# Performance work log

Hardware: AMD Instinct MI355X
Metric: run time of the kernel (lower is better)

Reference implementation:

```python
import jax, jax.numpy as jnp
import numpy as np

HEADS = 8
DIM_HEAD = 64


def setup_inputs() -> dict:
    key = jax.random.key(0)
    ks = jax.random.split(key, 7)
    b, c, h, w = 8, 256, 64, 64
    hidden = HEADS * DIM_HEAD  # 512
    return {
        "x": jax.random.normal(ks[0], (b, c, h, w), dtype=jnp.float32),
        "context": jax.random.normal(ks[1], (b, c, h, w), dtype=jnp.float32),
        "Wq": jax.random.normal(ks[2], (hidden, c), dtype=jnp.float32) * 0.02,
        "Wk": jax.random.normal(ks[3], (hidden, c), dtype=jnp.float32) * 0.02,
        "Wv": jax.random.normal(ks[4], (hidden, c), dtype=jnp.float32) * 0.02,
        "Wo": jax.random.normal(ks[5], (c, hidden), dtype=jnp.float32) * 0.02,
        "bo": jnp.zeros((c,), dtype=jnp.float32),
    }


def reference(x, context, Wq, Wk, Wv, Wo, bo):
    b, c, h, w = x.shape
    n = h * w
    scale = DIM_HEAD ** (-0.5)
    xf = x.reshape(b, c, n)                      # b c n
    cf = context.reshape(b, context.shape[1], -1)  # b c m
    # 1x1 convs == per-pixel linear projections
    q = jnp.einsum('bcn,oc->bon', xf, Wq).reshape(b, HEADS, DIM_HEAD, n) * scale
    k = jnp.einsum('bcm,oc->bom', cf, Wk).reshape(b, HEADS, DIM_HEAD, -1)
    v = jnp.einsum('bcm,oc->bom', cf, Wv).reshape(b, HEADS, DIM_HEAD, -1)
    k = jax.nn.softmax(k, axis=-1)               # softmax over spatial positions
    ctx = jnp.einsum('bhdm,bhem->bhde', k, v)    # small d x e context
    out = jnp.einsum('bhde,bhdn->bhen', ctx, q)  # b h e n
    out = out.reshape(b, HEADS * DIM_HEAD, h, w)
    return jnp.einsum('bchw,oc->bohw', out, Wo) + bo[None, :, None, None]
```

## Files before the change

### kernel.cpp

```cpp
#include <hip/hip_runtime.h>

#define B   8
#define C   256
#define N   4096
#define H   8
#define D   64
#define HID 512
#define SCALE 0.125f

typedef __attribute__((ext_vector_type(8))) __bf16 bf16x8;
typedef __attribute__((ext_vector_type(4))) float f32x4;

__device__ __forceinline__ ushort f2bf(float f) {
  union { float f; unsigned u; } v; v.f = f;
  unsigned r = v.u + 0x7FFFu + ((v.u >> 16) & 1u);
  return (ushort)(r >> 16);
}

__device__ __forceinline__ f32x4 mfma16(bf16x8 a, bf16x8 b, f32x4 c) {
  return __builtin_amdgcn_mfma_f32_16x16x32_bf16(a, b, c, 0, 0, 0);
}

__global__ __launch_bounds__(256) void cast_w_kernel(
    const float* __restrict__ Wk, const float* __restrict__ Wv,
    ushort* __restrict__ wk_bf, ushort* __restrict__ wv_bf) {
  const int t = (blockIdx.x * 256 + threadIdx.x) * 4;
  const float4 a = *(const float4*)(Wk + t);
  const float4 b = *(const float4*)(Wv + t);
  ushort4 ra, rb;
  ra.x = f2bf(a.x); ra.y = f2bf(a.y); ra.z = f2bf(a.z); ra.w = f2bf(a.w);
  rb.x = f2bf(b.x); rb.y = f2bf(b.y); rb.z = f2bf(b.z); rb.w = f2bf(b.w);
  *(ushort4*)(wk_bf + t) = ra;
  *(ushort4*)(wv_bf + t) = rb;
}

__global__ __launch_bounds__(256) void transpose_cast_kernel(
    const float* __restrict__ src, ushort* __restrict__ dst, int R, int L) {
  __shared__ float tile[64 * 65];
  const int l0 = blockIdx.x * 64, r0 = blockIdx.y * 64, b = blockIdx.z;
  const int tid = threadIdx.x;
  const int rr = tid >> 4, c4 = (tid & 15) << 2;
  const float* sp = src + ((size_t)b * R + r0) * L + l0;
#pragma unroll
  for (int p = 0; p < 4; ++p) {
    const float4 v = *(const float4*)(sp + (size_t)(rr + p * 16) * L + c4);
    float* tp = tile + (rr + p * 16) * 65 + c4;
    tp[0] = v.x; tp[1] = v.y; tp[2] = v.z; tp[3] = v.w;
  }
  __syncthreads();
  const int lr = tid >> 2, rb = (tid & 3) << 4;
  uint pk[8];
#pragma unroll
  for (int k = 0; k < 16; k += 2) {
    const uint lo = f2bf(tile[(rb + k) * 65 + lr]);
    const uint hi = f2bf(tile[(rb + k + 1) * 65 + lr]);
    pk[k >> 1] = lo | (hi << 16);
  }
  ushort* dp = dst + ((size_t)b * L + l0 + lr) * R + r0 + rb;
  *(uint4*)dp = *(uint4*)pk;
  *(uint4*)(dp + 8) = *(uint4*)(pk + 4);
}

__global__ __launch_bounds__(256, 3) void kv_mfma_kernel(
    const ushort* __restrict__ ctxt_bf,
    const ushort* __restrict__ wk_bf,
    const ushort* __restrict__ wv_bf,
    float* __restrict__ ctx_part,
    float* __restrict__ z_part)
{
  __shared__ __align__(16) ushort cb_s[64 * 256];
  __shared__ __align__(16) ushort p_s[64 * 64];
  __shared__ __align__(16) ushort v_s[64 * 64];
  const int mt = blockIdx.x, h = blockIdx.y, b = blockIdx.z;
  const int tid = threadIdx.x;
  const int w = tid >> 6, lane = tid & 63;
  const int col = lane & 15, quad = lane >> 4;
  const int dw = w * 16;
  const int c7 = col & 7;

  const ushort* wkp = wk_bf + (size_t)(h * 64 + dw + col) * C + quad * 8;
  const ushort* wvp = wv_bf + (size_t)(h * 64 + dw + col) * C + quad * 8;

  const int sgcol = lane & 31;
  const int srowo = w * 16 + (lane >> 5);

  const f32x4 z4 = {0.f, 0.f, 0.f, 0.f};
  f32x4 cacc[4];
#pragma unroll
  for (int j = 0; j < 4; ++j) cacc[j] = z4;
  float zl = 0.f;

  for (int mh = 0; mh < 4; ++mh) {
    const size_t m0 = (size_t)mt * 256 + mh * 64;
    const ushort* cbg = ctxt_bf + ((size_t)b * N + m0) * C;

#pragma unroll
    for (int it = 0; it < 8; ++it) {
      const int row = srowo + it * 2;
      const uint4 vld = *(const uint4*)(cbg + (size_t)row * C + sgcol * 8);
      const int gc = sgcol ^ (row & 7);
      *(uint4*)(cb_s + row * 256 + gc * 8) = vld;
    }
    __syncthreads();

    f32x4 kacc[4], vacc[4];
#pragma unroll
    for (int i = 0; i < 4; ++i) { kacc[i] = z4; vacc[i] = z4; }
#pragma unroll
    for (int kc = 0; kc < 2; ++kc) {
      bf16x8 wkf[4], wvf[4];
#pragma unroll
      for (int kk = 0; kk < 4; ++kk) {
        wkf[kk] = *(const bf16x8*)(wkp + (size_t)(kc * 4 + kk) * 32);
        wvf[kk] = *(const bf16x8*)(wvp + (size_t)(kc * 4 + kk) * 32);
      }
#pragma unroll
      for (int kk = 0; kk < 4; ++kk) {
        const int kg = (kc * 4 + kk) * 4 + quad;
        bf16x8 a[4];
#pragma unroll
        for (int i = 0; i < 4; ++i) {
          const int r = i * 16 + col;
          a[i] = *(const bf16x8*)(cb_s + r * 256 + (kg ^ (r & 7)) * 8);
        }
#pragma unroll
        for (int i = 0; i < 4; ++i) {
          kacc[i] = mfma16(a[i], wkf[kk], kacc[i]);
          vacc[i] = mfma16(a[i], wvf[kk], vacc[i]);
        }
      }
    }

#pragma unroll
    for (int i = 0; i < 4; ++i) {
      const int off = (dw + col) * 64 + (((i * 2 + (quad >> 1)) ^ c7) << 3) +
                      ((quad & 1) << 2);
      const f32x4 k4 = kacc[i];
      const float e0 = __expf(k4[0]), e1 = __expf(k4[1]);
      const float e2 = __expf(k4[2]), e3 = __expf(k4[3]);
      zl += (e0 + e1) + (e2 + e3);
      ushort4 pk; pk.x = f2bf(e0); pk.y = f2bf(e1);
      pk.z = f2bf(e2); pk.w = f2bf(e3);
      *(ushort4*)(p_s + off) = pk;
      const f32x4 v4 = vacc[i];
      ushort4 vk; vk.x = f2bf(v4[0]); vk.y = f2bf(v4[1]);
      vk.z = f2bf(v4[2]); vk.w = f2bf(v4[3]);
      *(ushort4*)(v_s + off) = vk;
    }
    __syncthreads();

#pragma unroll
    for (int kq = 0; kq < 2; ++kq) {
      const int gsw = ((kq * 4 + quad) ^ c7) << 3;
      const bf16x8 pa = *(const bf16x8*)(p_s + (dw + col) * 64 + gsw);
      bf16x8 vb[4];
#pragma unroll
      for (int j = 0; j < 4; ++j)
        vb[j] = *(const bf16x8*)(v_s + (j * 16 + col) * 64 + gsw);
#pragma unroll
      for (int j = 0; j < 4; ++j) cacc[j] = mfma16(pa, vb[j], cacc[j]);
    }
  }

  {
    float s = zl;
    s += __shfl_xor(s, 16); s += __shfl_xor(s, 32);
    if (quad == 0)
      z_part[((size_t)(b * H + h) * 16 + mt) * 64 + dw + col] = s;
  }

  float* outp = ctx_part + ((size_t)(b * H + h) * 16 + mt) * 4096;
#pragma unroll
  for (int j = 0; j < 4; ++j)
#pragma unroll
    for (int r = 0; r < 4; ++r)
      outp[(size_t)(dw + quad * 4 + r) * 64 + j * 16 + col] = cacc[j][r];
}

__global__ __launch_bounds__(256) void combine_kernel(
    const float* __restrict__ ctx_part, const float* __restrict__ z_part,
    float* __restrict__ ctxn)
{
  const int bh = blockIdx.x, seg = blockIdx.y, tid = threadIdx.x;
  __shared__ float zs[64];
  if (tid < 64) {
    float z = 0.f;
#pragma unroll
    for (int p = 0; p < 16; ++p) z += z_part[((size_t)bh * 16 + p) * 64 + tid];
    zs[tid] = SCALE / z;
  }
  __syncthreads();
  const int idx = (seg << 8) + tid;
  const float* cp = ctx_part + (size_t)bh * 16 * 4096;
  float s = 0.f;
#pragma unroll
  for (int p = 0; p < 16; ++p) s += cp[(size_t)p * 4096 + idx];
  ctxn[((size_t)bh << 12) + idx] = s * zs[idx >> 6];
}

__global__ __launch_bounds__(256) void a_kernel(
    const float* __restrict__ ctxn, const float* __restrict__ Wq,
    float* __restrict__ A)
{
  const int bh = blockIdx.x, cti = blockIdx.y, tid = threadIdx.x;
  const int b = bh >> 3, h = bh & 7;
  const int c0 = cti << 6;
  __shared__ float ct[64 * 65];
  __shared__ float wq[64 * 68];
  for (int r = 0; r < 16; ++r) {
    const int idx = tid + (r << 8);
    ct[(idx & 63) * 65 + (idx >> 6)] = ctxn[((size_t)bh << 12) + idx];
    wq[(idx >> 6) * 68 + (idx & 63)] =
        Wq[(size_t)(h * 64 + (idx >> 6)) * C + c0 + (idx & 63)];
  }
  __syncthreads();
  const int e = tid & 63, co = tid >> 6;
  float acc[16];
#pragma unroll
  for (int k = 0; k < 16; ++k) acc[k] = 0.f;
  for (int d = 0; d < 64; ++d) {
    const float cv = ct[e * 65 + d];
    const float* wr = wq + d * 68 + co * 16;
#pragma unroll
    for (int k = 0; k < 16; ++k) acc[k] += cv * wr[k];
  }
  float* Ar = A + ((size_t)b * HID + h * 64 + e) * C + c0 + co * 16;
#pragma unroll
  for (int k = 0; k < 16; ++k) Ar[k] = acc[k];
}

__global__ __launch_bounds__(256) void m_kernel(
    const float* __restrict__ A, const float* __restrict__ Wo,
    ushort* __restrict__ M_bf)
{
  const int tile = blockIdx.x, b = blockIdx.y;
  const int o0 = (tile & 7) << 5, c0 = (tile >> 3) << 6;
  const int tid = threadIdx.x, tx = tid & 15, ty = tid >> 4;
  __shared__ float wo_s[16 * 36];
  __shared__ float a_s[16 * 68];
  float acc[2][4] = {{0.f}};
  const int ow = tid >> 3, koff = (tid & 7) << 1;
  const int kk = tid >> 4, cc = (tid & 15) << 2;
  for (int k0 = 0; k0 < HID; k0 += 16) {
    __syncthreads();
    const float2 w2 = *(const float2*)(Wo + (size_t)(o0 + ow) * HID + k0 + koff);
    wo_s[(koff + 0) * 36 + ow] = w2.x;
    wo_s[(koff + 1) * 36 + ow] = w2.y;
    *(float4*)(a_s + kk * 68 + cc) =
        *(const float4*)(A + ((size_t)b * HID + k0 + kk) * C + c0 + cc);
    __syncthreads();
#pragma unroll
    for (int kc = 0; kc < 16; ++kc) {
      const float2 wv = *(const float2*)(wo_s + kc * 36 + ty * 2);
      const float4 av = *(const float4*)(a_s + kc * 68 + tx * 4);
      acc[0][0] += wv.x * av.x; acc[0][1] += wv.x * av.y;
      acc[0][2] += wv.x * av.z; acc[0][3] += wv.x * av.w;
      acc[1][0] += wv.y * av.x; acc[1][1] += wv.y * av.y;
      acc[1][2] += wv.y * av.z; acc[1][3] += wv.y * av.w;
    }
  }
#pragma unroll
  for (int i = 0; i < 2; ++i) {
    ushort4 r;
    r.x = f2bf(acc[i][0]); r.y = f2bf(acc[i][1]);
    r.z = f2bf(acc[i][2]); r.w = f2bf(acc[i][3]);
    *(ushort4*)(M_bf + ((size_t)b * C + o0 + ty * 2 + i) * C + c0 + tx * 4) = r;
  }
}

__global__ __launch_bounds__(256, 4) void out_mfma_kernel(
    const ushort* __restrict__ M_bf,
    const ushort* __restrict__ x_bf,
    const float* __restrict__ bo, float* __restrict__ out)
{
  const int nt = blockIdx.x, ot = blockIdx.y, b = blockIdx.z;
  const int tid = threadIdx.x;
  const int w = tid >> 6, lane = tid & 63;
  const int col = lane & 15, quad = lane >> 4;
  const int o0 = ot * 32;
  const size_t n_base = (size_t)nt * 256 + w * 64;
  const ushort* Ab = M_bf + ((size_t)b * C + o0 + col) * C + quad * 8;
  const ushort* Bb = x_bf + ((size_t)b * N + n_base) * C + quad * 8;

  const f32x4 z4 = {0.f, 0.f, 0.f, 0.f};
  f32x4 acc[2][4];
#pragma unroll
  for (int i = 0; i < 2; ++i)
#pragma unroll
    for (int j = 0; j < 4; ++j) acc[i][j] = z4;

#pragma unroll
  for (int kk = 0; kk < 8; ++kk) {
    bf16x8 af[2], bfz[4];
#pragma unroll
    for (int i = 0; i < 2; ++i)
      af[i] = *(const bf16x8*)(Ab + (size_t)(i * 16) * C + kk * 32);
#pragma unroll
    for (int j = 0; j < 4; ++j)
      bfz[j] = *(const bf16x8*)(Bb + (size_t)(j * 16 + col) * C + kk * 32);
#pragma unroll
    for (int i = 0; i < 2; ++i)
#pragma unroll
      for (int j = 0; j < 4; ++j) acc[i][j] = mfma16(af[i], bfz[j], acc[i][j]);
  }

#pragma unroll
  for (int i = 0; i < 2; ++i)
#pragma unroll
    for (int r = 0; r < 4; ++r) {
      const int o = o0 + i * 16 + quad * 4 + r;
      const float bias = bo[o];
      float* op = out + ((size_t)b * C + o) * N + n_base + col;
#pragma unroll
      for (int j = 0; j < 4; ++j) op[j * 16] = acc[i][j][r] + bias;
    }
}

extern "C" void kernel_launch(void* const* d_in, const int* in_sizes, int n_in,
                              void* d_out, int out_size, void* d_ws, size_t ws_size,
                              hipStream_t stream) {
  const float* x    = (const float*)d_in[0];
  const float* ctxt = (const float*)d_in[1];
  const float* Wq   = (const float*)d_in[2];
  const float* Wk   = (const float*)d_in[3];
  const float* Wv   = (const float*)d_in[4];
  const float* Wo   = (const float*)d_in[5];
  const float* bo   = (const float*)d_in[6];
  float* out = (float*)d_out;

  char* p = (char*)d_ws;
  ushort* ctxt_bf = (ushort*)p;  p += (size_t)B * N * C * 2;
  ushort* wk_bf   = (ushort*)p;  p += (size_t)HID * C * 2;
  ushort* wv_bf   = (ushort*)p;  p += (size_t)HID * C * 2;
  ushort* M_bf    = (ushort*)p;  p += (size_t)B * C * C * 2;
  float*  z_part  = (float*)p;   p += (size_t)B * H * 16 * 64 * 4;
  float*  ctxn    = (float*)p;   p += (size_t)B * H * D * D * 4;
  float*  ctx_part= (float*)p;   p += (size_t)B * H * 16 * 4096 * 4;
  float*  A       = ctx_part;
  ushort* x_bf    = ctxt_bf;

  cast_w_kernel<<<dim3(HID * C / 1024), 256, 0, stream>>>(Wk, Wv, wk_bf, wv_bf);
  transpose_cast_kernel<<<dim3(N / 64, C / 64, B), 256, 0, stream>>>(ctxt, ctxt_bf, C, N);
  kv_mfma_kernel<<<dim3(16, H, B), 256, 0, stream>>>(ctxt_bf, wk_bf, wv_bf, ctx_part, z_part);
  transpose_cast_kernel<<<dim3(N / 64, C / 64, B), 256, 0, stream>>>(x, x_bf, C, N);
  combine_kernel<<<dim3(B * H, 16), 256, 0, stream>>>(ctx_part, z_part, ctxn);
  a_kernel<<<dim3(B * H, 4), 256, 0, stream>>>(ctxn, Wq, A);
  m_kernel<<<dim3(32, B), 256, 0, stream>>>(A, Wo, M_bf);
  out_mfma_kernel<<<dim3(N / 256, C / 32, B), 256, 0, stream>>>(M_bf, x_bf, bo, out);
}
```

Measured before the change: 219.4 us.

## Merge prep casts into one launch and double-buffer KV tiles via direct LDS loads

Folds the weight cast and both transpose-casts into a single prep kernel launch, giving x its own bf16 buffer instead of reusing the context buffer. The KV projection kernel now works on 32-row tiles with double-buffered shared memory filled by global_load_lds, prefetching the next tile while computing the current one. Occupancy is raised to 4 blocks per SM. The aim is fewer launches and hiding global-load latency, at the cost of more workspace and an extra barrier per tile.

Result: no change. 218.0 us (-0.7%).

```diff
diff --git a/kernel.cpp b/kernel.cpp
--- a/kernel.cpp
+++ b/kernel.cpp
@@ -21,29 +21,42 @@
   return __builtin_amdgcn_mfma_f32_16x16x32_bf16(a, b, c, 0, 0, 0);
 }
 
-__global__ __launch_bounds__(256) void cast_w_kernel(
+__device__ __forceinline__ void glds16(const ushort* g, ushort* l) {
+  __builtin_amdgcn_global_load_lds(
+      (const __attribute__((address_space(1))) void*)g,
+      (__attribute__((address_space(3))) void*)l, 16, 0, 0);
+}
+
+__global__ __launch_bounds__(256) void prep_kernel(
+    const float* __restrict__ x, const float* __restrict__ ctxt,
     const float* __restrict__ Wk, const float* __restrict__ Wv,
+    ushort* __restrict__ x_bf, ushort* __restrict__ ctxt_bf,
     ushort* __restrict__ wk_bf, ushort* __restrict__ wv_bf) {
-  const int t = (blockIdx.x * 256 + threadIdx.x) * 4;
-  const float4 a = *(const float4*)(Wk + t);
-  const float4 b = *(const float4*)(Wv + t);
-  ushort4 ra, rb;
-  ra.x = f2bf(a.x); ra.y = f2bf(a.y); ra.z = f2bf(a.z); ra.w = f2bf(a.w);
-  rb.x = f2bf(b.x); rb.y = f2bf(b.y); rb.z = f2bf(b.z); rb.w = f2bf(b.w);
-  *(ushort4*)(wk_bf + t) = ra;
-  *(ushort4*)(wv_bf + t) = rb;
-}
-
-__global__ __launch_bounds__(256) void transpose_cast_kernel(
-    const float* __restrict__ src, ushort* __restrict__ dst, int R, int L) {
+  const int z = blockIdx.z;
+  if (z == 16) {
+    const int id = blockIdx.y * 64 + blockIdx.x;
+    if (id >= 128) return;
+    const int t = (id * 256 + threadIdx.x) * 4;
+    const float4 a = *(const float4*)(Wk + t);
+    const float4 b = *(const float4*)(Wv + t);
+    ushort4 ra, rb;
+    ra.x = f2bf(a.x); ra.y = f2bf(a.y); ra.z = f2bf(a.z); ra.w = f2bf(a.w);
+    rb.x = f2bf(b.x); rb.y = f2bf(b.y); rb.z = f2bf(b.z); rb.w = f2bf(b.w);
+    *(ushort4*)(wk_bf + t) = ra;
+    *(ushort4*)(wv_bf + t) = rb;
+    return;
+  }
   __shared__ float tile[64 * 65];
-  const int l0 = blockIdx.x * 64, r0 = blockIdx.y * 64, b = blockIdx.z;
+  const int b = z & 7;
+  const float* src = (z < 8) ? ctxt : x;
+  ushort* dst = (z < 8) ? ctxt_bf : x_bf;
+  const int l0 = blockIdx.x * 64, r0 = blockIdx.y * 64;
   const int tid = threadIdx.x;
   const int rr = tid >> 4, c4 = (tid & 15) << 2;
-  const float* sp = src + ((size_t)b * R + r0) * L + l0;
+  const float* sp = src + ((size_t)b * C + r0) * N + l0;
 #pragma unroll
   for (int p = 0; p < 4; ++p) {
-    const float4 v = *(const float4*)(sp + (size_t)(rr + p * 16) * L + c4);
+    const float4 v = *(const float4*)(sp + (size_t)(rr + p * 16) * N + c4);
     float* tp = tile + (rr + p * 16) * 65 + c4;
     tp[0] = v.x; tp[1] = v.y; tp[2] = v.z; tp[3] = v.w;
   }
@@ -56,33 +69,34 @@
     const uint hi = f2bf(tile[(rb + k + 1) * 65 + lr]);
     pk[k >> 1] = lo | (hi << 16);
   }
-  ushort* dp = dst + ((size_t)b * L + l0 + lr) * R + r0 + rb;
+  ushort* dp = dst + ((size_t)b * N + l0 + lr) * C + r0 + rb;
   *(uint4*)dp = *(uint4*)pk;
   *(uint4*)(dp + 8) = *(uint4*)(pk + 4);
 }
 
-__global__ __launch_bounds__(256, 3) void kv_mfma_kernel(
+__global__ __launch_bounds__(256, 4) void kv_mfma_kernel(
     const ushort* __restrict__ ctxt_bf,
     const ushort* __restrict__ wk_bf,
     const ushort* __restrict__ wv_bf,
     float* __restrict__ ctx_part,
     float* __restrict__ z_part)
 {
-  __shared__ __align__(16) ushort cb_s[64 * 256];
-  __shared__ __align__(16) ushort p_s[64 * 64];
-  __shared__ __align__(16) ushort v_s[64 * 64];
+  __shared__ __align__(16) ushort cb_s[2][32 * 256];
+  __shared__ __align__(16) ushort p_s[64 * 32];
+  __shared__ __align__(16) ushort v_s[64 * 32];
   const int mt = blockIdx.x, h = blockIdx.y, b = blockIdx.z;
   const int tid = threadIdx.x;
   const int w = tid >> 6, lane = tid & 63;
   const int col = lane & 15, quad = lane >> 4;
   const int dw = w * 16;
-  const int c7 = col & 7;
+  const int swc = (col & 3) ^ ((col >> 2) & 3);
 
   const ushort* wkp = wk_bf + (size_t)(h * 64 + dw + col) * C + quad * 8;
   const ushort* wvp = wv_bf + (size_t)(h * 64 + dw + col) * C + quad * 8;
-
-  const int sgcol = lane & 31;
-  const int srowo = w * 16 + (lane >> 5);
+  const ushort* cbase = ctxt_bf + ((size_t)b * N + (size_t)mt * 256) * C;
+
+  const int grow0 = w * 8 + (lane >> 5);
+  const int ggran = lane & 31;
 
   const f32x4 z4 = {0.f, 0.f, 0.f, 0.f};
   f32x4 cacc[4];
@@ -90,51 +104,51 @@
   for (int j = 0; j < 4; ++j) cacc[j] = z4;
   float zl = 0.f;
 
-  for (int mh = 0; mh < 4; ++mh) {
-    const size_t m0 = (size_t)mt * 256 + mh * 64;
-    const ushort* cbg = ctxt_bf + ((size_t)b * N + m0) * C;
-
-#pragma unroll
-    for (int it = 0; it < 8; ++it) {
-      const int row = srowo + it * 2;
-      const uint4 vld = *(const uint4*)(cbg + (size_t)row * C + sgcol * 8);
-      const int gc = sgcol ^ (row & 7);
-      *(uint4*)(cb_s + row * 256 + gc * 8) = vld;
-    }
-    __syncthreads();
-
-    f32x4 kacc[4], vacc[4];
-#pragma unroll
-    for (int i = 0; i < 4; ++i) { kacc[i] = z4; vacc[i] = z4; }
-#pragma unroll
-    for (int kc = 0; kc < 2; ++kc) {
-      bf16x8 wkf[4], wvf[4];
-#pragma unroll
-      for (int kk = 0; kk < 4; ++kk) {
-        wkf[kk] = *(const bf16x8*)(wkp + (size_t)(kc * 4 + kk) * 32);
-        wvf[kk] = *(const bf16x8*)(wvp + (size_t)(kc * 4 + kk) * 32);
+#pragma unroll
+  for (int it = 0; it < 4; ++it) {
+    const int row = grow0 + it * 2;
+    glds16(cbase + (size_t)row * C + ((ggran ^ (row & 7)) << 3),
+           &cb_s[0][(w * 8 + it * 2) * 256]);
+  }
+  __syncthreads();
+
+  for (int t = 0; t < 8; ++t) {
+    const int cur = t & 1;
+    if (t < 7) {
+      const ushort* nb = cbase + (size_t)(t + 1) * 32 * C;
+#pragma unroll
+      for (int it = 0; it < 4; ++it) {
+        const int row = grow0 + it * 2;
+        glds16(nb + (size_t)row * C + ((ggran ^ (row & 7)) << 3),
+               &cb_s[cur ^ 1][(w * 8 + it * 2) * 256]);
       }
-#pragma unroll
-      for (int kk = 0; kk < 4; ++kk) {
-        const int kg = (kc * 4 + kk) * 4 + quad;
-        bf16x8 a[4];
-#pragma unroll
-        for (int i = 0; i < 4; ++i) {
-          const int r = i * 16 + col;
-          a[i] = *(const bf16x8*)(cb_s + r * 256 + (kg ^ (r & 7)) * 8);
-        }
-#pragma unroll
-        for (int i = 0; i < 4; ++i) {
-          kacc[i] = mfma16(a[i], wkf[kk], kacc[i]);
-          vacc[i] = mfma16(a[i], wvf[kk], vacc[i]);
-        }
+    }
+
+    f32x4 kacc[2], vacc[2];
+#pragma unroll
+    for (int i = 0; i < 2; ++i) { kacc[i] = z4; vacc[i] = z4; }
+#pragma unroll
+    for (int kk = 0; kk < 8; ++kk) {
+      bf16x8 a[2];
+#pragma unroll
+      for (int i = 0; i < 2; ++i) {
+        const int r = i * 16 + col;
+        a[i] = *(const bf16x8*)(&cb_s[cur][r * 256 +
+                  ((((kk << 2) + quad) ^ (r & 7)) << 3)]);
       }
-    }
-
-#pragma unroll
-    for (int i = 0; i < 4; ++i) {
-      const int off = (dw + col) * 64 + (((i * 2 + (quad >> 1)) ^ c7) << 3) +
-                      ((quad & 1) << 2);
+      const bf16x8 wkf = *(const bf16x8*)(wkp + (size_t)kk * 32);
+      const bf16x8 wvf = *(const bf16x8*)(wvp + (size_t)kk * 32);
+#pragma unroll
+      for (int i = 0; i < 2; ++i) {
+        kacc[i] = mfma16(a[i], wkf, kacc[i]);
+        vacc[i] = mfma16(a[i], wvf, vacc[i]);
+      }
+    }
+
+#pragma unroll
+    for (int i = 0; i < 2; ++i) {
+      const int off = (dw + col) * 32 +
+                      (((i * 2 + (quad >> 1)) ^ swc) << 3) + ((quad & 1) << 2);
       const f32x4 k4 = kacc[i];
       const float e0 = __expf(k4[0]), e1 = __expf(k4[1]);
       const float e2 = __expf(k4[2]), e3 = __expf(k4[3]);
@@ -149,17 +163,17 @@
     }
     __syncthreads();
 
-#pragma unroll
-    for (int kq = 0; kq < 2; ++kq) {
-      const int gsw = ((kq * 4 + quad) ^ c7) << 3;
-      const bf16x8 pa = *(const bf16x8*)(p_s + (dw + col) * 64 + gsw);
+    {
+      const int g = (quad ^ swc) << 3;
+      const bf16x8 pa = *(const bf16x8*)(p_s + (dw + col) * 32 + g);
       bf16x8 vb[4];
 #pragma unroll
       for (int j = 0; j < 4; ++j)
-        vb[j] = *(const bf16x8*)(v_s + (j * 16 + col) * 64 + gsw);
+        vb[j] = *(const bf16x8*)(v_s + (j * 16 + col) * 32 + g);
 #pragma unroll
       for (int j = 0; j < 4; ++j) cacc[j] = mfma16(pa, vb[j], cacc[j]);
     }
+    __syncthreads();
   }
 
   {
@@ -330,6 +344,7 @@
 
   char* p = (char*)d_ws;
   ushort* ctxt_bf = (ushort*)p;  p += (size_t)B * N * C * 2;
+  ushort* x_bf    = (ushort*)p;  p += (size_t)B * N * C * 2;
   ushort* wk_bf   = (ushort*)p;  p += (size_t)HID * C * 2;
   ushort* wv_bf   = (ushort*)p;  p += (size_t)HID * C * 2;
   ushort* M_bf    = (ushort*)p;  p += (size_t)B * C * C * 2;
@@ -337,12 +352,10 @@
   float*  ctxn    = (float*)p;   p += (size_t)B * H * D * D * 4;
   float*  ctx_part= (float*)p;   p += (size_t)B * H * 16 * 4096 * 4;
   float*  A       = ctx_part;
-  ushort* x_bf    = ctxt_bf;
-
-  cast_w_kernel<<<dim3(HID * C / 1024), 256, 0, stream>>>(Wk, Wv, wk_bf, wv_bf);
-  transpose_cast_kernel<<<dim3(N / 64, C / 64, B), 256, 0, stream>>>(ctxt, ctxt_bf, C, N);
+
+  prep_kernel<<<dim3(N / 64, C / 64, 17), 256, 0, stream>>>(
+      x, ctxt, Wk, Wv, x_bf, ctxt_bf, wk_bf, wv_bf);
   kv_mfma_kernel<<<dim3(16, H, B), 256, 0, stream>>>(ctxt_bf, wk_bf, wv_bf, ctx_part, z_part);
-  transpose_cast_kernel<<<dim3(N / 64, C / 64, B), 256, 0, stream>>>(x, x_bf, C, N);
   combine_kernel<<<dim3(B * H, 16), 256, 0, stream>>>(ctx_part, z_part, ctxn);
   a_kernel<<<dim3(B * H, 4), 256, 0, stream>>>(ctxn, Wq, A);
   m_kernel<<<dim3(32, B), 256, 0, stream>>>(A, Wo, M_bf);
```
